# Optimization experiments

Hardware: AMD Instinct MI355X
Metric: run time of the kernel (lower is better)

The kernel has to match this reference:

```python
import jax, jax.numpy as jnp
from jax import lax
import numpy as np

B, N, P, NB = 64, 16, 20, 30      # frames, boxes/frame, num_persons, num_behaviors
C, F, OUT, SR = 1024, 14, 3, 2    # fmap channels, fmap size, roi output, sampling ratio
EPS = 1e-5


def roi_align_one(fmap, boxes):
    """fmap: [C,H,W]; boxes: [K,4]=(x1,y1,x2,y2) in fmap coords. Returns [K,C,OUT,OUT].
    torchvision-style roi_align (aligned=False) with fixed sampling_ratio=SR."""
    H, W = fmap.shape[1], fmap.shape[2]
    x1, y1, x2, y2 = boxes[:, 0], boxes[:, 1], boxes[:, 2], boxes[:, 3]
    rw = jnp.maximum(x2 - x1, 1.0)
    rh = jnp.maximum(y2 - y1, 1.0)
    S = OUT * SR
    pos = (jnp.arange(S, dtype=fmap.dtype) + 0.5) / SR            # sample pos in bin units
    ys = jnp.clip(y1[:, None] + pos[None, :] * (rh / OUT)[:, None], 0.0, H - 1.0)  # [K,S]
    xs = jnp.clip(x1[:, None] + pos[None, :] * (rw / OUT)[:, None], 0.0, W - 1.0)
    y0 = jnp.floor(ys); x0 = jnp.floor(xs)
    y0i = y0.astype(jnp.int32); x0i = x0.astype(jnp.int32)
    y1i = jnp.minimum(y0i + 1, H - 1); x1i = jnp.minimum(x0i + 1, W - 1)
    wy = ys - y0; wx = xs - x0                                     # [K,S]
    g = lambda yi, xi: fmap[:, yi[:, :, None], xi[:, None, :]]     # [C,K,S,S]
    v = (g(y0i, x0i) * ((1 - wy)[:, :, None] * (1 - wx)[:, None, :])
         + g(y0i, x1i) * ((1 - wy)[:, :, None] * wx[:, None, :])
         + g(y1i, x0i) * (wy[:, :, None] * (1 - wx)[:, None, :])
         + g(y1i, x1i) * (wy[:, :, None] * wx[:, None, :]))
    v = jnp.transpose(v, (1, 0, 2, 3))                             # [K,C,S,S]
    K = boxes.shape[0]
    return v.reshape(K, C, OUT, SR, OUT, SR).mean(axis=(3, 5))     # avg over samples


roi_align = jax.vmap(roi_align_one, in_axes=(0, 0))


def bn(x, g, b, m, v):
    s = (g / jnp.sqrt(v + EPS))[None, :, None, None]
    return x * s + (b - m * g / jnp.sqrt(v + EPS))[None, :, None, None]


def leaky(x):
    return jnp.where(x > 0, x, 0.1 * x)


def behavior_conv(x, w1, g1, b1, m1, v1, w2, g2, b2, m2, v2):
    dn = ('NCHW', 'OIHW', 'NCHW')
    x = lax.conv_general_dilated(x, w1, (1, 1), 'SAME', dimension_numbers=dn)
    x = leaky(bn(x, g1, b1, m1, v1))
    x = lax.conv_general_dilated(x, w2, (1, 1), 'SAME', dimension_numbers=dn)
    return leaky(bn(x, g2, b2, m2, v2))


def forward(fmap, boxes, conv1_w, bn1_g, bn1_b, bn1_m, bn1_v,
            conv2_w, bn2_g, bn2_b, bn2_m, bn2_v,
            conv1d_w, conv1d_b, fc1_w, fc1_b, fc2_w, fc2_b, person_idx):
    # --- global feature: ROI over the whole fmap per frame ---
    gbox = jnp.broadcast_to(jnp.array([[0.0, 0.0, F, F]], jnp.float32), (B, 1, 4))
    g_roi = roi_align(fmap, gbox).reshape(B, C, OUT, OUT)          # [B,1024,3,3]
    g_feat = behavior_conv(g_roi, conv1_w, bn1_g, bn1_b, bn1_m, bn1_v,
                           conv2_w, bn2_g, bn2_b, bn2_m, bn2_v)    # [B,256,3,3]
    g_feat = g_feat.reshape(B, 256 * OUT * OUT)                    # [B,2304]

    # --- per-box ROI features ---
    i_roi = roi_align(fmap, boxes).reshape(B * N, C, OUT, OUT)     # [B*N,1024,3,3]
    i_feat = behavior_conv(i_roi, conv1_w, bn1_g, bn1_b, bn1_m, bn1_v,
                           conv2_w, bn2_g, bn2_b, bn2_m, bn2_v)
    i_feat = i_feat.reshape(B, N, 256 * OUT * OUT)                 # [B,N,2304]

    # --- scatter-accumulate into behavior tensor [B,P,2304] ---
    behavior = jnp.broadcast_to(g_feat[:, None, :], (B, P, 2304))
    bidx = jnp.broadcast_to(jnp.arange(B)[:, None], (B, N))
    behavior = behavior.at[bidx, person_idx].add(i_feat)

    # --- temporal conv1d across the batch axis for every person slot ---
    x = jnp.transpose(behavior, (1, 2, 0))                         # [P,2304,B]
    x = lax.conv_general_dilated(x, conv1d_w, (1,), 'SAME',
                                 dimension_numbers=('NCH', 'OIH', 'NCH'))
    x = x + conv1d_b[None, :, None]                                # [P,2304,B]

    # --- gather each (frame, box)'s person feature at its frame and classify ---
    x = jnp.transpose(x, (2, 0, 1))                                # [B,P,2304]
    feats = jnp.take_along_axis(x, person_idx[:, :, None], axis=1) # [B,N,2304]
    h = jax.nn.relu(feats @ fc1_w + fc1_b)                         # dropout off (eval)
    return h @ fc2_w + fc2_b                                       # [B,N,NB]


def setup_inputs() -> dict:
    key = jax.random.key(0)
    ks = jax.random.split(key, 16)
    fmap = jax.random.normal(ks[0], (B, C, F, F), jnp.float32)
    lo = jax.random.uniform(ks[1], (B, N, 2), jnp.float32, 0.0, 9.0)
    sz = jax.random.uniform(ks[2], (B, N, 2), jnp.float32, 2.0, 5.0)
    hi = jnp.minimum(lo + sz, float(F))
    boxes = jnp.concatenate([lo, hi], axis=-1)                     # (x1,y1,x2,y2)
    person_idx = jax.random.randint(ks[3], (B, N), 0, P)
    s = lambda k, shape, fan: jax.random.normal(k, shape, jnp.float32) / np.sqrt(fan)
    return {
        'fmap': fmap, 'boxes': boxes, 'person_idx': person_idx,
        'conv1_w': s(ks[4], (512, 1024, 3, 3), 1024 * 9),
        'bn1_g': jnp.ones(512), 'bn1_b': jnp.zeros(512),
        'bn1_m': jnp.zeros(512), 'bn1_v': jnp.ones(512),
        'conv2_w': s(ks[5], (256, 512, 3, 3), 512 * 9),
        'bn2_g': jnp.ones(256), 'bn2_b': jnp.zeros(256),
        'bn2_m': jnp.zeros(256), 'bn2_v': jnp.ones(256),
        'conv1d_w': s(ks[6], (2304, 2304, 3), 2304 * 3),
        'conv1d_b': jnp.zeros(2304),
        'fc1_w': s(ks[7], (2304, 1024), 2304), 'fc1_b': jnp.zeros(1024),
        'fc2_w': s(ks[8], (1024, NB), 1024), 'fc2_b': jnp.zeros(NB),
    }


def reference(fmap, boxes, person_idx, conv1_w, bn1_g, bn1_b, bn1_m, bn1_v,
              conv2_w, bn2_g, bn2_b, bn2_m, bn2_v,
              conv1d_w, conv1d_b, fc1_w, fc1_b, fc2_w, fc2_b):
    return forward(fmap, boxes, conv1_w, bn1_g, bn1_b, bn1_m, bn1_v,
                   conv2_w, bn2_g, bn2_b, bn2_m, bn2_v,
                   conv1d_w, conv1d_b, fc1_w, fc1_b, fc2_w, fc2_b, person_idx)
```

## Files before the change

kernel.cpp:

```cpp
#include <hip/hip_runtime.h>
#include <hip/hip_bf16.h>
#include <cstdint>
#include <cstddef>

typedef __bf16 bf16;
typedef __bf16 bf16x8 __attribute__((ext_vector_type(8)));
typedef float f32x4 __attribute__((ext_vector_type(4)));

__device__ __forceinline__ void gload_lds16(const bf16* g, bf16* l) {
    __builtin_amdgcn_global_load_lds((const __attribute__((address_space(1))) void*)g,
                                     (__attribute__((address_space(3))) void*)l, 16, 0, 0);
}

template <int NT>
__global__ void __launch_bounds__(256) repack_w(const float* __restrict__ w, bf16* __restrict__ out,
                                                int OC, int IC) {
    int idx = blockIdx.x * 256 + threadIdx.x;
    if (idx >= OC * IC) return;
    int oc = idx / IC;
    int ic = idx - oc * IC;
    const float* src = w + (size_t)idx * NT;
    #pragma unroll
    for (int t = 0; t < NT; t++)
        out[(size_t)oc * NT * IC + t * IC + ic] = (bf16)src[t];
}

__global__ void __launch_bounds__(256) transpose_fc1(const float* __restrict__ w, bf16* __restrict__ out) {
    __shared__ float t[32][33];
    int iT = blockIdx.x * 32;
    int oT = blockIdx.y * 32;
    int tx = threadIdx.x, ty = threadIdx.y;
    #pragma unroll
    for (int j = 0; j < 4; j++)
        t[ty + j * 8][tx] = w[(size_t)(iT + ty + j * 8) * 1024 + oT + tx];
    __syncthreads();
    #pragma unroll
    for (int j = 0; j < 4; j++)
        out[(size_t)(oT + ty + j * 8) * 2304 + iT + tx] = (bf16)t[tx][ty + j * 8];
}

__global__ void __launch_bounds__(256) setup_all(int* __restrict__ rb1t, int* __restrict__ rb2t,
                                                 int* __restrict__ rb1dg, int* __restrict__ rbid,
                                                 int* __restrict__ tapmask,
                                                 const int* __restrict__ pidx,
                                                 bf16* __restrict__ zp1, bf16* __restrict__ zp2,
                                                 bf16* __restrict__ zp3,
                                                 const float* g1, const float* b1, const float* m1, const float* v1,
                                                 const float* g2, const float* b2, const float* m2, const float* v2,
                                                 float* __restrict__ s1, float* __restrict__ t1,
                                                 float* __restrict__ s2, float* __restrict__ t2,
                                                 const float* __restrict__ fc2_w, bf16* __restrict__ w2t) {
    int m = blockIdx.x * 256 + threadIdx.x;
    if (m < 9 * 9856) {
        int tap = m / 9856, r = m - tap * 9856;
        int mm = r < 9792 ? r : 0;
        int pos = mm / 1088, img = mm - pos * 1088;
        int oy = pos / 3, ox = pos - oy * 3;
        int ty = tap / 3, tx = tap - ty * 3;
        int iy = oy + ty - 1, ix = ox + tx - 1;
        bool valid = (iy >= 0) & (iy < 3) & (ix >= 0) & (ix < 3);
        int cell = iy * 3 + ix;
        rb1t[m] = valid ? 1024 + (img * 9 + cell) * 1024 : 0;
        rb2t[m] = valid ? 512 + (cell * 1088 + img) * 512 : 0;
    }
    if (m < 77) {
        int lo = (m * 128) / 1088;
        int hiRow = m * 128 + 127; if (hiRow > 9791) hiRow = 9791;
        int hi = hiRow / 1088;
        int msk = 0;
        for (int pos = lo; pos <= hi; ++pos) {
            int oy = pos / 3, ox = pos - oy * 3;
            int ym = oy == 0 ? 6 : (oy == 1 ? 7 : 3);
            int xm = ox == 0 ? 6 : (ox == 1 ? 7 : 3);
            #pragma unroll
            for (int ty = 0; ty < 3; ty++)
                #pragma unroll
                for (int tx = 0; tx < 3; tx++)
                    if (((ym >> ty) & 1) & ((xm >> tx) & 1))
                        msk |= 1 << (ty * 3 + tx);
        }
        tapmask[m] = msk;
    }
    if (m < 3 * 1024) {
        int tap = m / 1024, r = m - tap * 1024;
        int b = r >> 4;
        int p = pidx[r];
        int tt = b + tap - 1;
        bool valid = (tt >= 0) & (tt < 64);
        rb1dg[m] = valid ? 2304 + (p * 64 + tt) * 2304 : 0;
    }
    if (m < 1024) rbid[m] = m * 2304;
    if (m < 30 * 1024) {
        int n = m / 1024, k = m - n * 1024;
        w2t[m] = (bf16)fc2_w[(size_t)k * 30 + n];
    }
    if (m < 1024) zp1[m] = (bf16)0.f;
    if (m < 512)  zp2[m] = (bf16)0.f;
    if (m < 2304) zp3[m] = (bf16)0.f;
    if (m < 512) {
        float sc = g1[m] * rsqrtf(v1[m] + 1e-5f);
        s1[m] = sc; t1[m] = b1[m] - m1[m] * sc;
    } else if (m < 768) {
        int i = m - 512;
        float sc = g2[i] * rsqrtf(v2[i] + 1e-5f);
        s2[i] = sc; t2[i] = b2[i] - m2[i] * sc;
    }
}

__global__ void __launch_bounds__(256) transpose_fmap(const float* __restrict__ fmap, bf16* __restrict__ fml) {
    __shared__ float t[32][33];
    int img = blockIdx.z;
    int hwT = blockIdx.x * 32;
    int cT  = blockIdx.y * 32;
    int tx = threadIdx.x, ty = threadIdx.y;
    #pragma unroll
    for (int j = 0; j < 4; j++) {
        int c = cT + ty + j * 8;
        int hw = hwT + tx;
        if (hw < 196)
            t[ty + j * 8][tx] = fmap[((size_t)img * 1024 + c) * 196 + hw];
    }
    __syncthreads();
    #pragma unroll
    for (int j = 0; j < 4; j++) {
        int hw = hwT + ty + j * 8;
        int c = cT + tx;
        if (hw < 196)
            fml[((size_t)img * 196 + hw) * 1024 + c] = (bf16)t[tx][ty + j * 8];
    }
}

__global__ void __launch_bounds__(128) roi_kernel2(const bf16* __restrict__ fml, const float* __restrict__ boxes,
                                                   bf16* __restrict__ a1c) {
    int box = blockIdx.x;
    int tid = threadIdx.x;
    float x1, y1, x2, y2;
    int img;
    if (box < 64) { img = box; x1 = 0.f; y1 = 0.f; x2 = 14.f; y2 = 14.f; }
    else {
        int ib = box - 64;
        img = ib >> 4;
        const float* bb = boxes + (size_t)ib * 4;
        x1 = bb[0]; y1 = bb[1]; x2 = bb[2]; y2 = bb[3];
    }
    float rw = fmaxf(x2 - x1, 1.f), rh = fmaxf(y2 - y1, 1.f);
    __shared__ float swy[6], swx[6];
    __shared__ int sy0[6], sx0[6];
    if (tid < 6) {
        int i = tid;
        float pos = ((float)i + 0.5f) * 0.5f;
        float yv = fminf(fmaxf(y1 + pos * (rh * (1.f / 3.f)), 0.f), 13.f);
        float y0 = floorf(yv);
        sy0[i] = (int)y0; swy[i] = yv - y0;
        float xv = fminf(fmaxf(x1 + pos * (rw * (1.f / 3.f)), 0.f), 13.f);
        float x0 = floorf(xv);
        sx0[i] = (int)x0; swx[i] = xv - x0;
    }
    __syncthreads();
    const bf16* base = fml + (size_t)img * 196 * 1024 + tid * 8;
    #pragma unroll
    for (int oy = 0; oy < 3; oy++) {
        #pragma unroll
        for (int ox = 0; ox < 3; ox++) {
            float acc[8];
            #pragma unroll
            for (int e = 0; e < 8; e++) acc[e] = 0.f;
            #pragma unroll
            for (int dy = 0; dy < 2; dy++) {
                int sy = 2 * oy + dy;
                int y0 = sy0[sy]; float wy = swy[sy];
                int y1i = min(y0 + 1, 13);
                #pragma unroll
                for (int dx = 0; dx < 2; dx++) {
                    int sx = 2 * ox + dx;
                    int x0 = sx0[sx]; float wx = swx[sx];
                    int x1i = min(x0 + 1, 13);
                    bf16x8 f00 = *(const bf16x8*)(base + (size_t)(y0 * 14 + x0) * 1024);
                    bf16x8 f01 = *(const bf16x8*)(base + (size_t)(y0 * 14 + x1i) * 1024);
                    bf16x8 f10 = *(const bf16x8*)(base + (size_t)(y1i * 14 + x0) * 1024);
                    bf16x8 f11 = *(const bf16x8*)(base + (size_t)(y1i * 14 + x1i) * 1024);
                    float w00 = (1.f - wy) * (1.f - wx), w01 = (1.f - wy) * wx;
                    float w10 = wy * (1.f - wx),         w11 = wy * wx;
                    #pragma unroll
                    for (int e = 0; e < 8; e++)
                        acc[e] += w00 * (float)f00[e] + w01 * (float)f01[e]
                                + w10 * (float)f10[e] + w11 * (float)f11[e];
                }
            }
            bf16x8 o;
            #pragma unroll
            for (int e = 0; e < 8; e++) o[e] = (bf16)(acc[e] * 0.25f);
            *(bf16x8*)(a1c + 1024 + ((size_t)box * 9 + oy * 3 + ox) * 1024 + tid * 8) = o;
        }
    }
}

__global__ void __launch_bounds__(256) assemble(const float* __restrict__ feat, const int* __restrict__ pidx,
                                                bf16* __restrict__ asm3) {
    int b = blockIdx.x;
    int p = blockIdx.y;
    __shared__ int idxs[16];
    if (threadIdx.x < 16) idxs[threadIdx.x] = pidx[b * 16 + threadIdx.x];
    __syncthreads();
    const float* g = feat + (size_t)b * 2304;
    for (int f = threadIdx.x; f < 2304; f += 256) {
        float v = g[f];
        #pragma unroll
        for (int n = 0; n < 16; n++)
            if (idxs[n] == p) v += feat[(size_t)(64 + b * 16 + n) * 2304 + f];
        asm3[2304 + ((size_t)p * 64 + b) * 2304 + f] = (bf16)v;
    }
}

template <int MODE, int NSPLIT>
__global__ void __launch_bounds__(256) gemm_k(const bf16* __restrict__ A, const int* __restrict__ rowtab,
                                              const bf16* __restrict__ Bw, float* __restrict__ outp,
                                              const int* __restrict__ tapmask) {
    constexpr int K   = MODE == 0 ? 9216 : MODE == 1 ? 4608 : MODE == 2 ? 6912 : 2304;
    constexpr int N   = MODE == 0 ? 512  : MODE == 1 ? 256  : MODE == 2 ? 2304 : 1024;
    constexpr int Cin = MODE == 0 ? 1024 : MODE == 1 ? 512  : 2304;
    constexpr int M   = MODE <= 1 ? 9792 : 1024;
    constexpr int MT  = MODE <= 1 ? 9856 : 1024;
    constexpr bool MPAD = (M % 128) != 0;
    constexpr int KTS = (K / 64) / NSPLIT;

    const int bm = blockIdx.y * 128;
    const int bn = blockIdx.x * 128;
    const int z  = blockIdx.z;
    const int tid = threadIdx.x;
    const int lane = tid & 63, wave = tid >> 6;
    const int q = lane >> 4, ln16 = lane & 15;
    const int wr = wave >> 1, wc = wave & 1;

    __shared__ __align__(16) bf16 As[128 * 64];
    __shared__ __align__(16) bf16 Bs[128 * 64];

    const int sr = lane >> 3;
    const int sc = ((lane & 7) ^ sr) * 8;
    const bf16* gB[4];
    #pragma unroll
    for (int u = 0; u < 4; u++)
        gB[u] = Bw + (size_t)(bn + wave * 32 + u * 8 + sr) * K + sc;

    f32x4 acc[4][4];
    #pragma unroll
    for (int mt = 0; mt < 4; mt++)
        #pragma unroll
        for (int nt = 0; nt < 4; nt++)
            acc[mt][nt] = (f32x4){0.f, 0.f, 0.f, 0.f};

    if constexpr (MODE <= 1) {
        const int mask = tapmask[blockIdx.y];
        int ord = 0;
        for (int tap = 0; tap < 9; ++tap) {
            if (!((mask >> tap) & 1)) continue;
            if ((ord++) % NSPLIT != z) continue;
            int rbA[4];
            #pragma unroll
            for (int u = 0; u < 4; u++)
                rbA[u] = rowtab[tap * MT + bm + wave * 32 + u * 8 + sr];
            for (int kk = 0; kk < Cin / 64; ++kk) {
                const int aoff = kk * 64 + sc;
                const int k0 = tap * Cin + kk * 64;

                __syncthreads();
                #pragma unroll
                for (int u = 0; u < 4; u++)
                    gload_lds16(A + (size_t)(rbA[u] + aoff), As + (wave * 32 + u * 8) * 64);
                #pragma unroll
                for (int u = 0; u < 4; u++)
                    gload_lds16(gB[u] + k0, Bs + (wave * 32 + u * 8) * 64);
                __syncthreads();

                #pragma unroll
                for (int s = 0; s < 2; s++) {
                    bf16x8 af[4], bfr[4];
                    #pragma unroll
                    for (int mt = 0; mt < 4; mt++) {
                        int r = wr * 64 + mt * 16 + ln16;
                        af[mt] = *(const bf16x8*)(As + r * 64 + (((4 * s + q) ^ (ln16 & 7)) << 3));
                    }
                    #pragma unroll
                    for (int nt = 0; nt < 4; nt++) {
                        int r = wc * 64 + nt * 16 + ln16;
                        bfr[nt] = *(const bf16x8*)(Bs + r * 64 + (((4 * s + q) ^ (ln16 & 7)) << 3));
                    }
                    #pragma unroll
                    for (int mt = 0; mt < 4; mt++)
                        #pragma unroll
                        for (int nt = 0; nt < 4; nt++)
                            acc[mt][nt] = __builtin_amdgcn_mfma_f32_16x16x32_bf16(af[mt], bfr[nt], acc[mt][nt], 0, 0, 0);
                }
            }
        }
    } else {
        int rbA[4];
        int curtap = -1;
        for (int kt = z * KTS; kt < z * KTS + KTS; kt++) {
            const int k0 = kt * 64;
            const int tap = k0 / Cin;
            const int inner = k0 - tap * Cin;
            if (tap != curtap) {
                curtap = tap;
                #pragma unroll
                for (int u = 0; u < 4; u++)
                    rbA[u] = rowtab[tap * MT + bm + wave * 32 + u * 8 + sr];
            }
            const int aoff = inner + sc;

            __syncthreads();
            #pragma unroll
            for (int u = 0; u < 4; u++)
                gload_lds16(A + (size_t)(rbA[u] + aoff), As + (wave * 32 + u * 8) * 64);
            #pragma unroll
            for (int u = 0; u < 4; u++)
                gload_lds16(gB[u] + k0, Bs + (wave * 32 + u * 8) * 64);
            __syncthreads();

            #pragma unroll
            for (int s = 0; s < 2; s++) {
                bf16x8 af[4], bfr[4];
                #pragma unroll
                for (int mt = 0; mt < 4; mt++) {
                    int r = wr * 64 + mt * 16 + ln16;
                    af[mt] = *(const bf16x8*)(As + r * 64 + (((4 * s + q) ^ (ln16 & 7)) << 3));
                }
                #pragma unroll
                for (int nt = 0; nt < 4; nt++) {
                    int r = wc * 64 + nt * 16 + ln16;
                    bfr[nt] = *(const bf16x8*)(Bs + r * 64 + (((4 * s + q) ^ (ln16 & 7)) << 3));
                }
                #pragma unroll
                for (int mt = 0; mt < 4; mt++)
                    #pragma unroll
                    for (int nt = 0; nt < 4; nt++)
                        acc[mt][nt] = __builtin_amdgcn_mfma_f32_16x16x32_bf16(af[mt], bfr[nt], acc[mt][nt], 0, 0, 0);
            }
        }
    }

    #pragma unroll
    for (int mt = 0; mt < 4; mt++) {
        int gmBase = bm + wr * 64 + mt * 16 + q * 4;
        #pragma unroll
        for (int r = 0; r < 4; r++) {
            int gm = gmBase + r;
            if (MPAD && gm >= M) continue;
            #pragma unroll
            for (int nt = 0; nt < 4; nt++) {
                int gn = bn + wc * 64 + nt * 16 + ln16;
                outp[((size_t)z * M + gm) * N + gn] = acc[mt][nt][r];
            }
        }
    }
}

__global__ void __launch_bounds__(256) reduce0_tiled(const float* __restrict__ part,
                                                     float* __restrict__ feat,
                                                     const float* __restrict__ s2, const float* __restrict__ t2) {
    int c = blockIdx.x;
    int t = threadIdx.x;
    float acc[9];
    #pragma unroll
    for (int r = 0; r < 9; r++) acc[r] = 0.f;
    #pragma unroll
    for (int z = 0; z < 3; z++) {
        #pragma unroll
        for (int r = 0; r < 9; r++)
            acc[r] += part[((size_t)z * 9792 + r * 1088 + c) * 256 + t];
    }
    float s = s2[t], b = t2[t];
    __shared__ float L[9 * 257];
    #pragma unroll
    for (int r = 0; r < 9; r++) {
        float v = acc[r] * s + b;
        v = v > 0.f ? v : 0.1f * v;
        L[r * 257 + t] = v;
    }
    __syncthreads();
    float* fout = feat + (size_t)c * 2304;
    #pragma unroll
    for (int k = 0; k < 9; k++) {
        int f = t + k * 256;
        int oc = f / 9, pos = f - oc * 9;
        fout[f] = L[pos * 257 + oc];
    }
}

template <int RMODE>
__global__ void __launch_bounds__(256) reduce_k(const float* __restrict__ part, void* __restrict__ outp,
                                                const float* __restrict__ c0, const float* __restrict__ c1) {
    constexpr int M = RMODE == 1 ? 1024 : RMODE == 2 ? 1024 : 9792;
    constexpr int N = RMODE == 1 ? 2304 : RMODE == 2 ? 1024 : 512;
    constexpr int S = RMODE == 1 ? 4    : RMODE == 2 ? 6    : 3;
    int idx = blockIdx.x * 256 + threadIdx.x;
    if (idx >= M * N) return;
    int m = idx / N, n = idx - m * N;
    float v = 0.f;
    #pragma unroll
    for (int s = 0; s < S; s++) v += part[(size_t)s * M * N + idx];
    if constexpr (RMODE == 1) {
        v += c0[n];
        ((bf16*)outp)[idx] = (bf16)v;
    } else if constexpr (RMODE == 2) {
        v = fmaxf(v + c0[n], 0.f);
        ((bf16*)outp)[idx] = (bf16)v;
    } else {
        v = v * c0[n] + c1[n];
        v = v > 0.f ? v : 0.1f * v;
        ((bf16*)outp)[512 + (size_t)m * 512 + n] = (bf16)v;
    }
}

__global__ void __launch_bounds__(256) fc2_kernel(const bf16* __restrict__ h, const bf16* __restrict__ w2t,
                                                  const float* __restrict__ b2, float* __restrict__ out) {
    int tid = threadIdx.x;
    int m = blockIdx.x * 8 + (tid >> 5);
    int n = tid & 31;
    int n2 = n < 30 ? n : 29;
    const bf16* hr = h + (size_t)m * 1024;
    const bf16* wr = w2t + (size_t)n2 * 1024;
    float acc = 0.f;
    for (int k = 0; k < 1024; k += 8) {
        bf16x8 hv = *(const bf16x8*)(hr + k);
        bf16x8 wv = *(const bf16x8*)(wr + k);
        #pragma unroll
        for (int e = 0; e < 8; e++) acc += (float)hv[e] * (float)wv[e];
    }
    if (n < 30) out[(size_t)m * 30 + n] = acc + b2[n];
}

extern "C" void kernel_launch(void* const* d_in, const int* in_sizes, int n_in,
                              void* d_out, int out_size, void* d_ws, size_t ws_size,
                              hipStream_t stream) {
    const float* fmap     = (const float*)d_in[0];
    const float* boxes    = (const float*)d_in[1];
    const int*   pidx     = (const int*)d_in[2];
    const float* conv1_w  = (const float*)d_in[3];
    const float* bn1_g    = (const float*)d_in[4];
    const float* bn1_b    = (const float*)d_in[5];
    const float* bn1_m    = (const float*)d_in[6];
    const float* bn1_v    = (const float*)d_in[7];
    const float* conv2_w  = (const float*)d_in[8];
    const float* bn2_g    = (const float*)d_in[9];
    const float* bn2_b    = (const float*)d_in[10];
    const float* bn2_m    = (const float*)d_in[11];
    const float* bn2_v    = (const float*)d_in[12];
    const float* conv1d_w = (const float*)d_in[13];
    const float* conv1d_b = (const float*)d_in[14];
    const float* fc1_w    = (const float*)d_in[15];
    const float* fc1_b    = (const float*)d_in[16];
    const float* fc2_w    = (const float*)d_in[17];
    const float* fc2_b    = (const float*)d_in[18];
    float* out = (float*)d_out;

    char* ws = (char*)d_ws;

    float* s1    = (float*)(ws + 0);
    float* t1    = (float*)(ws + 2048);
    float* s2    = (float*)(ws + 4096);
    float* t2    = (float*)(ws + 5120);
    int*   rbid  = (int*)(ws + 6144);
    int*   rb1dg = (int*)(ws + 10240);
    int*   tapm  = (int*)(ws + 22528);
    int*   rb1t  = (int*)(ws + 25600);
    int*   rb2t  = (int*)(ws + 380416);
    bf16*  fml    = (bf16*)(ws + 768000);
    float* part1  = (float*)(ws + 768000);
    float* part2  = (float*)(ws + 768000);
    float* part1d = (float*)(ws + 768000);
    float* partfc = (float*)(ws + 768000);
    bf16*  a1c    = (bf16*)(ws + 60930048);
    bf16*  wb1d   = (bf16*)(ws + 60930048);
    bf16*  fc1t   = (bf16*)(ws + 92780544);
    bf16*  xbuf   = (bf16*)(ws + 97499136);
    bf16*  hbuf   = (bf16*)(ws + 102217728);
    bf16*  w2t    = (bf16*)(ws + 104314880);
    bf16*  wb1    = (bf16*)(ws + 104857600);
    bf16*  wb2    = (bf16*)(ws + 114294784);
    bf16*  a2c    = (bf16*)(ws + 116654080);
    bf16*  asm3   = (bf16*)(ws + 126682112);
    float* feat   = (float*)(ws + 132584960);

    bf16* zp1 = a1c;
    bf16* zp2 = a2c;
    bf16* zp3 = asm3;

    setup_all<<<(9 * 9856 + 255) / 256, 256, 0, stream>>>(rb1t, rb2t, rb1dg, rbid, tapm, pidx,
                                                          zp1, zp2, zp3,
                                                          bn1_g, bn1_b, bn1_m, bn1_v,
                                                          bn2_g, bn2_b, bn2_m, bn2_v,
                                                          s1, t1, s2, t2, fc2_w, w2t);
    repack_w<9><<<(512 * 1024 + 255) / 256, 256, 0, stream>>>(conv1_w, wb1, 512, 1024);
    repack_w<9><<<(256 * 512 + 255) / 256, 256, 0, stream>>>(conv2_w, wb2, 256, 512);

    transpose_fmap<<<dim3(7, 32, 64), dim3(32, 8), 0, stream>>>(fmap, fml);
    roi_kernel2<<<1088, 128, 0, stream>>>(fml, boxes, a1c);

    gemm_k<0, 3><<<dim3(4, 77, 3), 256, 0, stream>>>(a1c, rb1t, wb1, part1, tapm);
    reduce_k<3><<<(9792 * 512 + 255) / 256, 256, 0, stream>>>(part1, a2c, s1, t1);

    repack_w<3><<<(2304 * 2304 + 255) / 256, 256, 0, stream>>>(conv1d_w, wb1d, 2304, 2304);
    transpose_fc1<<<dim3(72, 32), dim3(32, 8), 0, stream>>>(fc1_w, fc1t);

    gemm_k<1, 3><<<dim3(2, 77, 3), 256, 0, stream>>>(a2c, rb2t, wb2, part2, tapm);
    reduce0_tiled<<<1088, 256, 0, stream>>>(part2, feat, s2, t2);
    assemble<<<dim3(64, 20), 256, 0, stream>>>(feat, pidx, asm3);
    gemm_k<2, 4><<<dim3(18, 8, 4), 256, 0, stream>>>(asm3, rb1dg, wb1d, part1d, tapm);
    reduce_k<1><<<(1024 * 2304 + 255) / 256, 256, 0, stream>>>(part1d, xbuf, conv1d_b, nullptr);
    gemm_k<3, 6><<<dim3(8, 8, 6), 256, 0, stream>>>(xbuf, rbid, fc1t, partfc, tapm);
    reduce_k<2><<<(1024 * 1024 + 255) / 256, 256, 0, stream>>>(partfc, hbuf, fc1_b, nullptr);
    fc2_kernel<<<128, 256, 0, stream>>>(hbuf, w2t, fc2_b, out);
    (void)in_sizes; (void)n_in; (void)out_size; (void)ws_size;
}
```

Baseline: 473.2 us.

## Use persistent atomic work queue with sorted tasks for conv GEMMs

The two conv GEMMs now launch 512 persistent blocks that pull tile tasks from an atomic counter. Tasks come from a list built in setup, ordered by descending number of active taps, so the heaviest tiles are scheduled first and load imbalance from the tap masks is reduced. The conv2 split count goes from 3 to 5 and the conv1d split count from 4 to 6, with the matching reductions updated. This adds atomic and synchronisation overhead per task, plus more partial-sum traffic for the larger splits.

```diff
diff --git a/kernel.cpp b/kernel.cpp
--- a/kernel.cpp
+++ b/kernel.cpp
@@ -10,6 +10,34 @@
 __device__ __forceinline__ void gload_lds16(const bf16* g, bf16* l) {
     __builtin_amdgcn_global_load_lds((const __attribute__((address_space(1))) void*)g,
                                      (__attribute__((address_space(3))) void*)l, 16, 0, 0);
+}
+
+__device__ __forceinline__ int block_tap_mask(int y) {
+    int lo = (y * 128) / 1088;
+    int hiRow = y * 128 + 127; if (hiRow > 9791) hiRow = 9791;
+    int hi = hiRow / 1088;
+    int msk = 0;
+    for (int pos = lo; pos <= hi; ++pos) {
+        int oy = pos / 3, ox = pos - oy * 3;
+        int ym = oy == 0 ? 6 : (oy == 1 ? 7 : 3);
+        int xm = ox == 0 ? 6 : (ox == 1 ? 7 : 3);
+        #pragma unroll
+        for (int ty = 0; ty < 3; ty++)
+            #pragma unroll
+            for (int tx = 0; tx < 3; tx++)
+                if (((ym >> ty) & 1) & ((xm >> tx) & 1))
+                    msk |= 1 << (ty * 3 + tx);
+    }
+    return msk;
+}
+
+__device__ __forceinline__ int ztap_count(int y, int z, int ns) {
+    int msk = block_tap_mask(y);
+    int c = 0, ord = 0;
+    #pragma unroll
+    for (int t = 0; t < 9; ++t)
+        if ((msk >> t) & 1) { if (ord % ns == z) c++; ord++; }
+    return c;
 }
 
 template <int NT>
@@ -42,6 +70,8 @@
 __global__ void __launch_bounds__(256) setup_all(int* __restrict__ rb1t, int* __restrict__ rb2t,
                                                  int* __restrict__ rb1dg, int* __restrict__ rbid,
                                                  int* __restrict__ tapmask,
+                                                 int* __restrict__ tasks1, int* __restrict__ tasks2,
+                                                 int* __restrict__ ctr,
                                                  const int* __restrict__ pidx,
                                                  bf16* __restrict__ zp1, bf16* __restrict__ zp2,
                                                  bf16* __restrict__ zp3,
@@ -63,23 +93,31 @@
         rb1t[m] = valid ? 1024 + (img * 9 + cell) * 1024 : 0;
         rb2t[m] = valid ? 512 + (cell * 1088 + img) * 512 : 0;
     }
-    if (m < 77) {
-        int lo = (m * 128) / 1088;
-        int hiRow = m * 128 + 127; if (hiRow > 9791) hiRow = 9791;
-        int hi = hiRow / 1088;
-        int msk = 0;
-        for (int pos = lo; pos <= hi; ++pos) {
-            int oy = pos / 3, ox = pos - oy * 3;
-            int ym = oy == 0 ? 6 : (oy == 1 ? 7 : 3);
-            int xm = ox == 0 ? 6 : (ox == 1 ? 7 : 3);
-            #pragma unroll
-            for (int ty = 0; ty < 3; ty++)
-                #pragma unroll
-                for (int tx = 0; tx < 3; tx++)
-                    if (((ym >> ty) & 1) & ((xm >> tx) & 1))
-                        msk |= 1 << (ty * 3 + tx);
+    if (m < 77) tapmask[m] = block_tap_mask(m);
+    if (blockIdx.x == 0) {
+        __shared__ int cnt3[231], cnt5[385];
+        for (int e = threadIdx.x; e < 231; e += 256) cnt3[e] = ztap_count(e / 3, e % 3, 3);
+        for (int e = threadIdx.x; e < 385; e += 256) cnt5[e] = ztap_count(e / 5, e % 5, 5);
+        __syncthreads();
+        for (int e = threadIdx.x; e < 231; e += 256) {
+            int c = cnt3[e], rank = 0;
+            for (int e2 = 0; e2 < 231; ++e2)
+                rank += (cnt3[e2] > c) | ((cnt3[e2] == c) & (e2 < e));
+            int y = e / 3, z = e - (e / 3) * 3;
+            int pk = (y << 5) | (z << 2);
+            #pragma unroll
+            for (int nt = 0; nt < 4; ++nt) tasks1[rank * 4 + nt] = pk | nt;
         }
-        tapmask[m] = msk;
+        for (int e = threadIdx.x; e < 385; e += 256) {
+            int c = cnt5[e], rank = 0;
+            for (int e2 = 0; e2 < 385; ++e2)
+                rank += (cnt5[e2] > c) | ((cnt5[e2] == c) & (e2 < e));
+            int y = e / 5, z = e - (e / 5) * 5;
+            int pk = (y << 5) | (z << 2);
+            #pragma unroll
+            for (int nt = 0; nt < 2; ++nt) tasks2[rank * 2 + nt] = pk | nt;
+        }
+        if (threadIdx.x == 0) { ctr[0] = 0; ctr[1] = 0; }
     }
     if (m < 3 * 1024) {
         int tap = m / 1024, r = m - tap * 1024;
@@ -215,7 +253,8 @@
 template <int MODE, int NSPLIT>
 __global__ void __launch_bounds__(256) gemm_k(const bf16* __restrict__ A, const int* __restrict__ rowtab,
                                               const bf16* __restrict__ Bw, float* __restrict__ outp,
-                                              const int* __restrict__ tapmask) {
+                                              const int* __restrict__ tapmask,
+                                              const int* __restrict__ tasklist, int* __restrict__ ctr) {
     constexpr int K   = MODE == 0 ? 9216 : MODE == 1 ? 4608 : MODE == 2 ? 6912 : 2304;
     constexpr int N   = MODE == 0 ? 512  : MODE == 1 ? 256  : MODE == 2 ? 2304 : 1024;
     constexpr int Cin = MODE == 0 ? 1024 : MODE == 1 ? 512  : 2304;
@@ -224,9 +263,6 @@
     constexpr bool MPAD = (M % 128) != 0;
     constexpr int KTS = (K / 64) / NSPLIT;
 
-    const int bm = blockIdx.y * 128;
-    const int bn = blockIdx.x * 128;
-    const int z  = blockIdx.z;
     const int tid = threadIdx.x;
     const int lane = tid & 63, wave = tid >> 6;
     const int q = lane >> 4, ln16 = lane & 15;
@@ -237,63 +273,109 @@
 
     const int sr = lane >> 3;
     const int sc = ((lane & 7) ^ sr) * 8;
-    const bf16* gB[4];
-    #pragma unroll
-    for (int u = 0; u < 4; u++)
-        gB[u] = Bw + (size_t)(bn + wave * 32 + u * 8 + sr) * K + sc;
-
-    f32x4 acc[4][4];
-    #pragma unroll
-    for (int mt = 0; mt < 4; mt++)
-        #pragma unroll
-        for (int nt = 0; nt < 4; nt++)
-            acc[mt][nt] = (f32x4){0.f, 0.f, 0.f, 0.f};
 
     if constexpr (MODE <= 1) {
-        const int mask = tapmask[blockIdx.y];
-        int ord = 0;
-        for (int tap = 0; tap < 9; ++tap) {
-            if (!((mask >> tap) & 1)) continue;
-            if ((ord++) % NSPLIT != z) continue;
-            int rbA[4];
+        constexpr int NT    = MODE == 0 ? 4 : 2;
+        constexpr int NTASK = (MODE == 0 ? 231 : 385) * NT;
+        int* stask = (int*)As;
+        for (;;) {
+            __syncthreads();
+            if (tid == 0) *stask = atomicAdd(ctr, 1);
+            __syncthreads();
+            const int T = *stask;
+            if (T >= NTASK) break;
+            const int pk = tasklist[T];
+            const int y = pk >> 5, zz = (pk >> 2) & 7, nt = pk & 3;
+            const int bm = y * 128, bn = nt * 128;
+
+            const bf16* gB[4];
             #pragma unroll
             for (int u = 0; u < 4; u++)
-                rbA[u] = rowtab[tap * MT + bm + wave * 32 + u * 8 + sr];
-            for (int kk = 0; kk < Cin / 64; ++kk) {
-                const int aoff = kk * 64 + sc;
-                const int k0 = tap * Cin + kk * 64;
-
-                __syncthreads();
+                gB[u] = Bw + (size_t)(bn + wave * 32 + u * 8 + sr) * K + sc;
+
+            f32x4 acc[4][4];
+            #pragma unroll
+            for (int mt = 0; mt < 4; mt++)
+                #pragma unroll
+                for (int nn = 0; nn < 4; nn++)
+                    acc[mt][nn] = (f32x4){0.f, 0.f, 0.f, 0.f};
+
+            const int mask = tapmask[y];
+            int ord = 0;
+            for (int tap = 0; tap < 9; ++tap) {
+                if (!((mask >> tap) & 1)) continue;
+                if ((ord++) % NSPLIT != zz) continue;
+                int rbA[4];
                 #pragma unroll
                 for (int u = 0; u < 4; u++)
-                    gload_lds16(A + (size_t)(rbA[u] + aoff), As + (wave * 32 + u * 8) * 64);
-                #pragma unroll
-                for (int u = 0; u < 4; u++)
-                    gload_lds16(gB[u] + k0, Bs + (wave * 32 + u * 8) * 64);
-                __syncthreads();
-
-                #pragma unroll
-                for (int s = 0; s < 2; s++) {
-                    bf16x8 af[4], bfr[4];
+                    rbA[u] = rowtab[tap * MT + bm + wave * 32 + u * 8 + sr];
+                for (int kk = 0; kk < Cin / 64; ++kk) {
+                    const int aoff = kk * 64 + sc;
+                    const int k0 = tap * Cin + kk * 64;
+
+                    __syncthreads();
                     #pragma unroll
-                    for (int mt = 0; mt < 4; mt++) {
-                        int r = wr * 64 + mt * 16 + ln16;
-                        af[mt] = *(const bf16x8*)(As + r * 64 + (((4 * s + q) ^ (ln16 & 7)) << 3));
+                    for (int u = 0; u < 4; u++)
+                        gload_lds16(A + (size_t)(rbA[u] + aoff), As + (wave * 32 + u * 8) * 64);
+                    #pragma unroll
+                    for (int u = 0; u < 4; u++)
+                        gload_lds16(gB[u] + k0, Bs + (wave * 32 + u * 8) * 64);
+                    __syncthreads();
+
+                    #pragma unroll
+                    for (int s = 0; s < 2; s++) {
+                        bf16x8 af[4], bfr[4];
+                        #pragma unroll
+                        for (int mt = 0; mt < 4; mt++) {
+                            int r = wr * 64 + mt * 16 + ln16;
+                            af[mt] = *(const bf16x8*)(As + r * 64 + (((4 * s + q) ^ (ln16 & 7)) << 3));
+                        }
+                        #pragma unroll
+                        for (int nn = 0; nn < 4; nn++) {
+                            int r = wc * 64 + nn * 16 + ln16;
+                            bfr[nn] = *(const bf16x8*)(Bs + r * 64 + (((4 * s + q) ^ (ln16 & 7)) << 3));
+                        }
+                        #pragma unroll
+                        for (int mt = 0; mt < 4; mt++)
+                            #pragma unroll
+                            for (int nn = 0; nn < 4; nn++)
+                                acc[mt][nn] = __builtin_amdgcn_mfma_f32_16x16x32_bf16(af[mt], bfr[nn], acc[mt][nn], 0, 0, 0);
                     }
+                }
+            }
+
+            #pragma unroll
+            for (int mt = 0; mt < 4; mt++) {
+                int gmBase = bm + wr * 64 + mt * 16 + q * 4;
+                #pragma unroll
+                for (int r = 0; r < 4; r++) {
+                    int gm = gmBase + r;
+                    if (gm >= M) continue;
                     #pragma unroll
-                    for (int nt = 0; nt < 4; nt++) {
-                        int r = wc * 64 + nt * 16 + ln16;
-                        bfr[nt] = *(const bf16x8*)(Bs + r * 64 + (((4 * s + q) ^ (ln16 & 7)) << 3));
+                    for (int nn = 0; nn < 4; nn++) {
+                        int gn = bn + wc * 64 + nn * 16 + ln16;
+                        outp[((size_t)zz * M + gm) * N + gn] = acc[mt][nn][r];
                     }
-                    #pragma unroll
-                    for (int mt = 0; mt < 4; mt++)
-                        #pragma unroll
-                        for (int nt = 0; nt < 4; nt++)
-                            acc[mt][nt] = __builtin_amdgcn_mfma_f32_16x16x32_bf16(af[mt], bfr[nt], acc[mt][nt], 0, 0, 0);
                 }
             }
         }
     } else {
+        const int bm = blockIdx.y * 128;
+        const int bn = blockIdx.x * 128;
+        const int z  = blockIdx.z;
+
+        const bf16* gB[4];
+        #pragma unroll
+        for (int u = 0; u < 4; u++)
+            gB[u] = Bw + (size_t)(bn + wave * 32 + u * 8 + sr) * K + sc;
+
+        f32x4 acc[4][4];
+        #pragma unroll
+        for (int mt = 0; mt < 4; mt++)
+            #pragma unroll
+            for (int nn = 0; nn < 4; nn++)
+                acc[mt][nn] = (f32x4){0.f, 0.f, 0.f, 0.f};
+
         int rbA[4];
         int curtap = -1;
         for (int kt = z * KTS; kt < z * KTS + KTS; kt++) {
@@ -326,30 +408,30 @@
                     af[mt] = *(const bf16x8*)(As + r * 64 + (((4 * s + q) ^ (ln16 & 7)) << 3));
                 }
                 #pragma unroll
-                for (int nt = 0; nt < 4; nt++) {
-                    int r = wc * 64 + nt * 16 + ln16;
-                    bfr[nt] = *(const bf16x8*)(Bs + r * 64 + (((4 * s + q) ^ (ln16 & 7)) << 3));
+                for (int nn = 0; nn < 4; nn++) {
+                    int r = wc * 64 + nn * 16 + ln16;
+                    bfr[nn] = *(const bf16x8*)(Bs + r * 64 + (((4 * s + q) ^ (ln16 & 7)) << 3));
                 }
                 #pragma unroll
                 for (int mt = 0; mt < 4; mt++)
                     #pragma unroll
-                    for (int nt = 0; nt < 4; nt++)
-                        acc[mt][nt] = __builtin_amdgcn_mfma_f32_16x16x32_bf16(af[mt], bfr[nt], acc[mt][nt], 0, 0, 0);
+                    for (int nn = 0; nn < 4; nn++)
+                        acc[mt][nn] = __builtin_amdgcn_mfma_f32_16x16x32_bf16(af[mt], bfr[nn], acc[mt][nn], 0, 0, 0);
             }
         }
-    }
-
-    #pragma unroll
-    for (int mt = 0; mt < 4; mt++) {
-        int gmBase = bm + wr * 64 + mt * 16 + q * 4;
-        #pragma unroll
-        for (int r = 0; r < 4; r++) {
-            int gm = gmBase + r;
-            if (MPAD && gm >= M) continue;
-            #pragma unroll
-            for (int nt = 0; nt < 4; nt++) {
-                int gn = bn + wc * 64 + nt * 16 + ln16;
-                outp[((size_t)z * M + gm) * N + gn] = acc[mt][nt][r];
+
+        #pragma unroll
+        for (int mt = 0; mt < 4; mt++) {
+            int gmBase = bm + wr * 64 + mt * 16 + q * 4;
+            #pragma unroll
+            for (int r = 0; r < 4; r++) {
+                int gm = gmBase + r;
+                if (MPAD && gm >= M) continue;
+                #pragma unroll
+                for (int nn = 0; nn < 4; nn++) {
+                    int gn = bn + wc * 64 + nn * 16 + ln16;
+                    outp[((size_t)z * M + gm) * N + gn] = acc[mt][nn][r];
+                }
             }
         }
     }
@@ -364,7 +446,7 @@
     #pragma unroll
     for (int r = 0; r < 9; r++) acc[r] = 0.f;
     #pragma unroll
-    for (int z = 0; z < 3; z++) {
+    for (int z = 0; z < 5; z++) {
         #pragma unroll
         for (int r = 0; r < 9; r++)
             acc[r] += part[((size_t)z * 9792 + r * 1088 + c) * 256 + t];
@@ -392,7 +474,7 @@
                                                 const float* __restrict__ c0, const float* __restrict__ c1) {
     constexpr int M = RMODE == 1 ? 1024 : RMODE == 2 ? 1024 : 9792;
     constexpr int N = RMODE == 1 ? 2304 : RMODE == 2 ? 1024 : 512;
-    constexpr int S = RMODE == 1 ? 4    : RMODE == 2 ? 6    : 3;
+    constexpr int S = RMODE == 1 ? 6    : RMODE == 2 ? 6    : 3;
     int idx = blockIdx.x * 256 + threadIdx.x;
     if (idx >= M * N) return;
     int m = idx / N, n = idx - m * N;
@@ -465,6 +547,9 @@
     int*   tapm  = (int*)(ws + 22528);
     int*   rb1t  = (int*)(ws + 25600);
     int*   rb2t  = (int*)(ws + 380416);
+    int*   tasks1 = (int*)(ws + 735232);
+    int*   tasks2 = (int*)(ws + 738944);
+    int*   ctr    = (int*)(ws + 742400);
     bf16*  fml    = (bf16*)(ws + 768000);
     float* part1  = (float*)(ws + 768000);
     float* part2  = (float*)(ws + 768000);
@@ -486,7 +571,8 @@
     bf16* zp2 = a2c;
     bf16* zp3 = asm3;
 
-    setup_all<<<(9 * 9856 + 255) / 256, 256, 0, stream>>>(rb1t, rb2t, rb1dg, rbid, tapm, pidx,
+    setup_all<<<(9 * 9856 + 255) / 256, 256, 0, stream>>>(rb1t, rb2t, rb1dg, rbid, tapm,
+                                                          tasks1, tasks2, ctr, pidx,
                                                           zp1, zp2, zp3,
                                                           bn1_g, bn1_b, bn1_m, bn1_v,
                                                           bn2_g, bn2_b, bn2_m, bn2_v,
@@ -497,18 +583,18 @@
     transpose_fmap<<<dim3(7, 32, 64), dim3(32, 8), 0, stream>>>(fmap, fml);
     roi_kernel2<<<1088, 128, 0, stream>>>(fml, boxes, a1c);
 
-    gemm_k<0, 3><<<dim3(4, 77, 3), 256, 0, stream>>>(a1c, rb1t, wb1, part1, tapm);
+    gemm_k<0, 3><<<512, 256, 0, stream>>>(a1c, rb1t, wb1, part1, tapm, tasks1, ctr);
     reduce_k<3><<<(9792 * 512 + 255) / 256, 256, 0, stream>>>(part1, a2c, s1, t1);
 
     repack_w<3><<<(2304 * 2304 + 255) / 256, 256, 0, stream>>>(conv1d_w, wb1d, 2304, 2304);
     transpose_fc1<<<dim3(72, 32), dim3(32, 8), 0, stream>>>(fc1_w, fc1t);
 
-    gemm_k<1, 3><<<dim3(2, 77, 3), 256, 0, stream>>>(a2c, rb2t, wb2, part2, tapm);
+    gemm_k<1, 5><<<512, 256, 0, stream>>>(a2c, rb2t, wb2, part2, tapm, tasks2, ctr + 1);
     reduce0_tiled<<<1088, 256, 0, stream>>>(part2, feat, s2, t2);
     assemble<<<dim3(64, 20), 256, 0, stream>>>(feat, pidx, asm3);
-    gemm_k<2, 4><<<dim3(18, 8, 4), 256, 0, stream>>>(asm3, rb1dg, wb1d, part1d, tapm);
+    gemm_k<2, 6><<<dim3(18, 8, 6), 256, 0, stream>>>(asm3, rb1dg, wb1d, part1d, tapm, nullptr, nullptr);
     reduce_k<1><<<(1024 * 2304 + 255) / 256, 256, 0, stream>>>(part1d, xbuf, conv1d_b, nullptr);
-    gemm_k<3, 6><<<dim3(8, 8, 6), 256, 0, stream>>>(xbuf, rbid, fc1t, partfc, tapm);
+    gemm_k<3, 6><<<dim3(8, 8, 6), 256, 0, stream>>>(xbuf, rbid, fc1t, partfc, tapm, nullptr, nullptr);
     reduce_k<2><<<(1024 * 1024 + 255) / 256, 256, 0, stream>>>(partfc, hbuf, fc1_b, nullptr);
     fc2_kernel<<<128, 256, 0, stream>>>(hbuf, w2t, fc2_b, out);
     (void)in_sizes; (void)n_in; (void)out_size; (void)ws_size;
```

After: 495.1 us. 1.05x slower.

## Schedule conv GEMMs via balanced task list with variable split-K per row block

Applied to the files above, without the earlier changes.

Replaces the fixed 3D grid for the two 3x3 conv GEMMs with a 1D task list built in setup. Each row block gets ceil(taps/3) splits and tasks are sorted heaviest first. This drops empty split blocks and meant to balance work across CUs. Reductions now read only the third partial where it exists, which cuts partial-buffer traffic. The cost is a serial O(n^2) ranking step in setup block 0 and some extra index math in the reduces.

```diff
diff --git a/kernel.cpp b/kernel.cpp
--- a/kernel.cpp
+++ b/kernel.cpp
@@ -10,6 +10,25 @@
 __device__ __forceinline__ void gload_lds16(const bf16* g, bf16* l) {
     __builtin_amdgcn_global_load_lds((const __attribute__((address_space(1))) void*)g,
                                      (__attribute__((address_space(3))) void*)l, 16, 0, 0);
+}
+
+__device__ __forceinline__ int block_tap_mask(int y) {
+    int lo = (y * 128) / 1088;
+    int hiRow = y * 128 + 127; if (hiRow > 9791) hiRow = 9791;
+    int hi = hiRow / 1088;
+    int msk = 0;
+    for (int pos = lo; pos <= hi; ++pos) {
+        int oy = pos / 3, ox = pos - oy * 3;
+        int ym = oy == 0 ? 6 : (oy == 1 ? 7 : 3);
+        int xm = ox == 0 ? 6 : (ox == 1 ? 7 : 3);
+        #pragma unroll
+        for (int ty = 0; ty < 3; ty++)
+            #pragma unroll
+            for (int tx = 0; tx < 3; tx++)
+                if (((ym >> ty) & 1) & ((xm >> tx) & 1))
+                    msk |= 1 << (ty * 3 + tx);
+    }
+    return msk;
 }
 
 template <int NT>
@@ -42,6 +61,7 @@
 __global__ void __launch_bounds__(256) setup_all(int* __restrict__ rb1t, int* __restrict__ rb2t,
                                                  int* __restrict__ rb1dg, int* __restrict__ rbid,
                                                  int* __restrict__ tapmask,
+                                                 int* __restrict__ tasks1, int* __restrict__ tasks2,
                                                  const int* __restrict__ pidx,
                                                  bf16* __restrict__ zp1, bf16* __restrict__ zp2,
                                                  bf16* __restrict__ zp3,
@@ -63,23 +83,40 @@
         rb1t[m] = valid ? 1024 + (img * 9 + cell) * 1024 : 0;
         rb2t[m] = valid ? 512 + (cell * 1088 + img) * 512 : 0;
     }
-    if (m < 77) {
-        int lo = (m * 128) / 1088;
-        int hiRow = m * 128 + 127; if (hiRow > 9791) hiRow = 9791;
-        int hi = hiRow / 1088;
-        int msk = 0;
-        for (int pos = lo; pos <= hi; ++pos) {
-            int oy = pos / 3, ox = pos - oy * 3;
-            int ym = oy == 0 ? 6 : (oy == 1 ? 7 : 3);
-            int xm = ox == 0 ? 6 : (ox == 1 ? 7 : 3);
-            #pragma unroll
-            for (int ty = 0; ty < 3; ty++)
-                #pragma unroll
-                for (int tx = 0; tx < 3; tx++)
-                    if (((ym >> ty) & 1) & ((xm >> tx) & 1))
-                        msk |= 1 << (ty * 3 + tx);
-        }
-        tapmask[m] = msk;
+    if (m < 77) tapmask[m] = block_tap_mask(m);
+    if (blockIdx.x == 0) {
+        __shared__ int sJ[77], sBase[78];
+        __shared__ int ey[164], ej[164], ew[164];
+        int t = threadIdx.x;
+        if (t < 77) sJ[t] = (__popc(block_tap_mask(t)) + 2) / 3;
+        __syncthreads();
+        if (t == 0) {
+            int acc = 0;
+            for (int y = 0; y < 77; ++y) { sBase[y] = acc; acc += sJ[y]; }
+            sBase[77] = acc;
+        }
+        __syncthreads();
+        if (t < 77) {
+            int T = __popc(block_tap_mask(t));
+            int J = sJ[t];
+            int w[3] = {0, 0, 0};
+            for (int o = 0; o < T; ++o) w[o * J / T]++;
+            for (int jj = 0; jj < J; ++jj) {
+                int e = sBase[t] + jj;
+                ey[e] = t; ej[e] = jj; ew[e] = w[jj];
+            }
+        }
+        __syncthreads();
+        if (t < 164) {
+            int wv = ew[t], rank = 0;
+            for (int e2 = 0; e2 < 164; ++e2)
+                rank += (ew[e2] > wv) | ((ew[e2] == wv) & (e2 < t));
+            int pk = (ey[t] << 5) | (ej[t] << 2);
+            #pragma unroll
+            for (int nt = 0; nt < 4; ++nt) tasks1[rank * 4 + nt] = pk | nt;
+            #pragma unroll
+            for (int nt = 0; nt < 2; ++nt) tasks2[rank * 2 + nt] = pk | nt;
+        }
     }
     if (m < 3 * 1024) {
         int tap = m / 1024, r = m - tap * 1024;
@@ -215,7 +252,8 @@
 template <int MODE, int NSPLIT>
 __global__ void __launch_bounds__(256) gemm_k(const bf16* __restrict__ A, const int* __restrict__ rowtab,
                                               const bf16* __restrict__ Bw, float* __restrict__ outp,
-                                              const int* __restrict__ tapmask) {
+                                              const int* __restrict__ tapmask,
+                                              const int* __restrict__ tasklist) {
     constexpr int K   = MODE == 0 ? 9216 : MODE == 1 ? 4608 : MODE == 2 ? 6912 : 2304;
     constexpr int N   = MODE == 0 ? 512  : MODE == 1 ? 256  : MODE == 2 ? 2304 : 1024;
     constexpr int Cin = MODE == 0 ? 1024 : MODE == 1 ? 512  : 2304;
@@ -224,9 +262,6 @@
     constexpr bool MPAD = (M % 128) != 0;
     constexpr int KTS = (K / 64) / NSPLIT;
 
-    const int bm = blockIdx.y * 128;
-    const int bn = blockIdx.x * 128;
-    const int z  = blockIdx.z;
     const int tid = threadIdx.x;
     const int lane = tid & 63, wave = tid >> 6;
     const int q = lane >> 4, ln16 = lane & 15;
@@ -237,6 +272,24 @@
 
     const int sr = lane >> 3;
     const int sc = ((lane & 7) ^ sr) * 8;
+
+    int bm, bn, z;
+    int mask = 0, T = 0, J = 0, jsel = 0;
+    if constexpr (MODE <= 1) {
+        const int pk = tasklist[blockIdx.x];
+        const int y = pk >> 5;
+        jsel = (pk >> 2) & 7;
+        const int nt = pk & 3;
+        bm = y * 128; bn = nt * 128; z = jsel;
+        mask = tapmask[y];
+        T = __popc(mask);
+        J = (T + 2) / 3;
+    } else {
+        bm = blockIdx.y * 128;
+        bn = blockIdx.x * 128;
+        z = blockIdx.z;
+    }
+
     const bf16* gB[4];
     #pragma unroll
     for (int u = 0; u < 4; u++)
@@ -246,15 +299,15 @@
     #pragma unroll
     for (int mt = 0; mt < 4; mt++)
         #pragma unroll
-        for (int nt = 0; nt < 4; nt++)
-            acc[mt][nt] = (f32x4){0.f, 0.f, 0.f, 0.f};
+        for (int nn = 0; nn < 4; nn++)
+            acc[mt][nn] = (f32x4){0.f, 0.f, 0.f, 0.f};
 
     if constexpr (MODE <= 1) {
-        const int mask = tapmask[blockIdx.y];
         int ord = 0;
         for (int tap = 0; tap < 9; ++tap) {
             if (!((mask >> tap) & 1)) continue;
-            if ((ord++) % NSPLIT != z) continue;
+            const int o = ord++;
+            if (o * J / T != jsel) continue;
             int rbA[4];
             #pragma unroll
             for (int u = 0; u < 4; u++)
@@ -281,15 +334,15 @@
                         af[mt] = *(const bf16x8*)(As + r * 64 + (((4 * s + q) ^ (ln16 & 7)) << 3));
                     }
                     #pragma unroll
-                    for (int nt = 0; nt < 4; nt++) {
-                        int r = wc * 64 + nt * 16 + ln16;
-                        bfr[nt] = *(const bf16x8*)(Bs + r * 64 + (((4 * s + q) ^ (ln16 & 7)) << 3));
+                    for (int nn = 0; nn < 4; nn++) {
+                        int r = wc * 64 + nn * 16 + ln16;
+                        bfr[nn] = *(const bf16x8*)(Bs + r * 64 + (((4 * s + q) ^ (ln16 & 7)) << 3));
                     }
                     #pragma unroll
                     for (int mt = 0; mt < 4; mt++)
                         #pragma unroll
-                        for (int nt = 0; nt < 4; nt++)
-                            acc[mt][nt] = __builtin_amdgcn_mfma_f32_16x16x32_bf16(af[mt], bfr[nt], acc[mt][nt], 0, 0, 0);
+                        for (int nn = 0; nn < 4; nn++)
+                            acc[mt][nn] = __builtin_amdgcn_mfma_f32_16x16x32_bf16(af[mt], bfr[nn], acc[mt][nn], 0, 0, 0);
                 }
             }
         }
@@ -326,15 +379,15 @@
                     af[mt] = *(const bf16x8*)(As + r * 64 + (((4 * s + q) ^ (ln16 & 7)) << 3));
                 }
                 #pragma unroll
-                for (int nt = 0; nt < 4; nt++) {
-                    int r = wc * 64 + nt * 16 + ln16;
-                    bfr[nt] = *(const bf16x8*)(Bs + r * 64 + (((4 * s + q) ^ (ln16 & 7)) << 3));
+                for (int nn = 0; nn < 4; nn++) {
+                    int r = wc * 64 + nn * 16 + ln16;
+                    bfr[nn] = *(const bf16x8*)(Bs + r * 64 + (((4 * s + q) ^ (ln16 & 7)) << 3));
                 }
                 #pragma unroll
                 for (int mt = 0; mt < 4; mt++)
                     #pragma unroll
-                    for (int nt = 0; nt < 4; nt++)
-                        acc[mt][nt] = __builtin_amdgcn_mfma_f32_16x16x32_bf16(af[mt], bfr[nt], acc[mt][nt], 0, 0, 0);
+                    for (int nn = 0; nn < 4; nn++)
+                        acc[mt][nn] = __builtin_amdgcn_mfma_f32_16x16x32_bf16(af[mt], bfr[nn], acc[mt][nn], 0, 0, 0);
             }
         }
     }
@@ -347,9 +400,9 @@
             int gm = gmBase + r;
             if (MPAD && gm >= M) continue;
             #pragma unroll
-            for (int nt = 0; nt < 4; nt++) {
-                int gn = bn + wc * 64 + nt * 16 + ln16;
-                outp[((size_t)z * M + gm) * N + gn] = acc[mt][nt][r];
+            for (int nn = 0; nn < 4; nn++) {
+                int gn = bn + wc * 64 + nn * 16 + ln16;
+                outp[((size_t)z * M + gm) * N + gn] = acc[mt][nn][r];
             }
         }
     }
@@ -357,17 +410,20 @@
 
 __global__ void __launch_bounds__(256) reduce0_tiled(const float* __restrict__ part,
                                                      float* __restrict__ feat,
-                                                     const float* __restrict__ s2, const float* __restrict__ t2) {
+                                                     const float* __restrict__ s2, const float* __restrict__ t2,
+                                                     const int* __restrict__ tapm) {
     int c = blockIdx.x;
     int t = threadIdx.x;
     float acc[9];
     #pragma unroll
-    for (int r = 0; r < 9; r++) acc[r] = 0.f;
-    #pragma unroll
-    for (int z = 0; z < 3; z++) {
-        #pragma unroll
-        for (int r = 0; r < 9; r++)
-            acc[r] += part[((size_t)z * 9792 + r * 1088 + c) * 256 + t];
+    for (int r = 0; r < 9; r++) {
+        int m = r * 1088 + c;
+        int y = m >> 7;
+        int J = (__popc(tapm[y]) + 2) / 3;
+        const float* p0 = part + (size_t)m * 256 + t;
+        float v = p0[0] + p0[(size_t)9792 * 256];
+        if (J == 3) v += p0[(size_t)2 * 9792 * 256];
+        acc[r] = v;
     }
     float s = s2[t], b = t2[t];
     __shared__ float L[9 * 257];
@@ -389,10 +445,11 @@
 
 template <int RMODE>
 __global__ void __launch_bounds__(256) reduce_k(const float* __restrict__ part, void* __restrict__ outp,
-                                                const float* __restrict__ c0, const float* __restrict__ c1) {
+                                                const float* __restrict__ c0, const float* __restrict__ c1,
+                                                const int* __restrict__ tapm) {
     constexpr int M = RMODE == 1 ? 1024 : RMODE == 2 ? 1024 : 9792;
     constexpr int N = RMODE == 1 ? 2304 : RMODE == 2 ? 1024 : 512;
-    constexpr int S = RMODE == 1 ? 4    : RMODE == 2 ? 6    : 3;
+    constexpr int S = RMODE == 1 ? 4    : RMODE == 2 ? 6    : 2;
     int idx = blockIdx.x * 256 + threadIdx.x;
     if (idx >= M * N) return;
     int m = idx / N, n = idx - m * N;
@@ -406,6 +463,9 @@
         v = fmaxf(v + c0[n], 0.f);
         ((bf16*)outp)[idx] = (bf16)v;
     } else {
+        int y = m >> 7;
+        int J = (__popc(tapm[y]) + 2) / 3;
+        if (J == 3) v += part[(size_t)2 * M * N + idx];
         v = v * c0[n] + c1[n];
         v = v > 0.f ? v : 0.1f * v;
         ((bf16*)outp)[512 + (size_t)m * 512 + n] = (bf16)v;
@@ -465,6 +525,8 @@
     int*   tapm  = (int*)(ws + 22528);
     int*   rb1t  = (int*)(ws + 25600);
     int*   rb2t  = (int*)(ws + 380416);
+    int*   tasks1 = (int*)(ws + 735232);
+    int*   tasks2 = (int*)(ws + 738944);
     bf16*  fml    = (bf16*)(ws + 768000);
     float* part1  = (float*)(ws + 768000);
     float* part2  = (float*)(ws + 768000);
@@ -486,7 +548,8 @@
     bf16* zp2 = a2c;
     bf16* zp3 = asm3;
 
-    setup_all<<<(9 * 9856 + 255) / 256, 256, 0, stream>>>(rb1t, rb2t, rb1dg, rbid, tapm, pidx,
+    setup_all<<<(9 * 9856 + 255) / 256, 256, 0, stream>>>(rb1t, rb2t, rb1dg, rbid, tapm,
+                                                          tasks1, tasks2, pidx,
                                                           zp1, zp2, zp3,
                                                           bn1_g, bn1_b, bn1_m, bn1_v,
                                                           bn2_g, bn2_b, bn2_m, bn2_v,
@@ -497,19 +560,19 @@
     transpose_fmap<<<dim3(7, 32, 64), dim3(32, 8), 0, stream>>>(fmap, fml);
     roi_kernel2<<<1088, 128, 0, stream>>>(fml, boxes, a1c);
 
-    gemm_k<0, 3><<<dim3(4, 77, 3), 256, 0, stream>>>(a1c, rb1t, wb1, part1, tapm);
-    reduce_k<3><<<(9792 * 512 + 255) / 256, 256, 0, stream>>>(part1, a2c, s1, t1);
+    gemm_k<0, 3><<<656, 256, 0, stream>>>(a1c, rb1t, wb1, part1, tapm, tasks1);
+    reduce_k<3><<<(9792 * 512 + 255) / 256, 256, 0, stream>>>(part1, a2c, s1, t1, tapm);
 
     repack_w<3><<<(2304 * 2304 + 255) / 256, 256, 0, stream>>>(conv1d_w, wb1d, 2304, 2304);
     transpose_fc1<<<dim3(72, 32), dim3(32, 8), 0, stream>>>(fc1_w, fc1t);
 
-    gemm_k<1, 3><<<dim3(2, 77, 3), 256, 0, stream>>>(a2c, rb2t, wb2, part2, tapm);
-    reduce0_tiled<<<1088, 256, 0, stream>>>(part2, feat, s2, t2);
+    gemm_k<1, 3><<<328, 256, 0, stream>>>(a2c, rb2t, wb2, part2, tapm, tasks2);
+    reduce0_tiled<<<1088, 256, 0, stream>>>(part2, feat, s2, t2, tapm);
     assemble<<<dim3(64, 20), 256, 0, stream>>>(feat, pidx, asm3);
-    gemm_k<2, 4><<<dim3(18, 8, 4), 256, 0, stream>>>(asm3, rb1dg, wb1d, part1d, tapm);
-    reduce_k<1><<<(1024 * 2304 + 255) / 256, 256, 0, stream>>>(part1d, xbuf, conv1d_b, nullptr);
-    gemm_k<3, 6><<<dim3(8, 8, 6), 256, 0, stream>>>(xbuf, rbid, fc1t, partfc, tapm);
-    reduce_k<2><<<(1024 * 1024 + 255) / 256, 256, 0, stream>>>(partfc, hbuf, fc1_b, nullptr);
+    gemm_k<2, 4><<<dim3(18, 8, 4), 256, 0, stream>>>(asm3, rb1dg, wb1d, part1d, tapm, nullptr);
+    reduce_k<1><<<(1024 * 2304 + 255) / 256, 256, 0, stream>>>(part1d, xbuf, conv1d_b, nullptr, nullptr);
+    gemm_k<3, 6><<<dim3(8, 8, 6), 256, 0, stream>>>(xbuf, rbid, fc1t, partfc, tapm, nullptr);
+    reduce_k<2><<<(1024 * 1024 + 255) / 256, 256, 0, stream>>>(partfc, hbuf, fc1_b, nullptr, nullptr);
     fc2_kernel<<<128, 256, 0, stream>>>(hbuf, w2t, fc2_b, out);
     (void)in_sizes; (void)n_in; (void)out_size; (void)ws_size;
 }
```

Result: faster. 456.5 us (-3.5%).
